# Kernel tuning notes

Measured on AMD Instinct MI355X. Metric: run time of the kernel, lower is better.

## Reference

```python
import jax, jax.numpy as jnp
import numpy as np

N, E, FN, FE, H, B = 8192, 32768, 32, 16, 73, 64
T_MP, T_S2S = 3, 12


def setup_inputs() -> dict:
    key = jax.random.key(0)
    k = jax.random.split(key, 24)
    s = 0.1
    p = lambda i, shape: jax.random.normal(k[i], shape, jnp.float32) * s
    return {
        "node_feats": jax.random.normal(k[0], (N, FN), jnp.float32),
        "edge_feats": jax.random.normal(k[1], (E, FE), jnp.float32),
        "W_in": p(2, (FN, H)), "b_in": p(3, (H,)),
        "ee_W1": p(4, (FE, H)), "ee_b1": p(5, (H,)),
        "ee_W2": p(6, (H, H * H)), "ee_b2": p(7, (H * H,)),
        "gru_Wih": p(8, (3 * H, H)), "gru_Whh": p(9, (3 * H, H)),
        "gru_bih": p(10, (3 * H,)), "gru_bhh": p(11, (3 * H,)),
        "lstm_Wih": p(12, (4 * H, 2 * H)), "lstm_Whh": p(13, (4 * H, H)),
        "lstm_bih": p(14, (4 * H,)), "lstm_bhh": p(15, (4 * H,)),
        "W_out": p(16, (H, 1)), "b_out": p(17, (1,)),
        "Esrc": jax.random.randint(k[18], (E,), 0, N),
        "Etgt": jax.random.randint(k[19], (E,), 0, N),
        "batch": jnp.sort(jax.random.randint(k[20], (N,), 0, B)),
    }


def reference(node_feats, edge_feats, W_in, b_in, ee_W1, ee_b1, ee_W2, ee_b2,
              gru_Wih, gru_Whh, gru_bih, gru_bhh,
              lstm_Wih, lstm_Whh, lstm_bih, lstm_bhh, W_out, b_out,
              Esrc, Etgt, batch):
    # EdgeEncoderMLP: edge features -> per-edge HxH weight matrices (Gilmer edge network)
    A = (jax.nn.relu(edge_feats @ ee_W1 + ee_b1) @ ee_W2 + ee_b2).reshape(E, H, H)
    h = node_feats @ W_in + b_in  # [N, H]

    def mp_step(h, _):
        m = jnp.einsum('eij,ej->ei', A, h[Esrc])           # per-edge matvec (gather-matmul)
        agg = jax.ops.segment_sum(m, Etgt, num_segments=N)  # scatter-add to targets
        # GRUCell update (torch gate order r,z,n)
        gi = agg @ gru_Wih.T + gru_bih
        gh = h @ gru_Whh.T + gru_bhh
        ir, iz, inn = jnp.split(gi, 3, axis=-1)
        hr, hz, hn = jnp.split(gh, 3, axis=-1)
        r = jax.nn.sigmoid(ir + hr)
        z = jax.nn.sigmoid(iz + hz)
        n = jnp.tanh(inn + r * hn)
        return (1.0 - z) * n + z * h, None

    h, _ = jax.lax.scan(mp_step, h, None, length=T_MP)

    # Set2Set pooling with a 1-layer LSTM (torch gate order i,f,g,o)
    def s2s_step(carry, _):
        q_star, hh, cc = carry
        gates = q_star @ lstm_Wih.T + lstm_bih + hh @ lstm_Whh.T + lstm_bhh
        i, f, g, o = jnp.split(gates, 4, axis=-1)
        cc = jax.nn.sigmoid(f) * cc + jax.nn.sigmoid(i) * jnp.tanh(g)
        hh = jax.nn.sigmoid(o) * jnp.tanh(cc)
        q = hh                                              # [B, H]
        e = jnp.sum(h * q[batch], axis=-1)                  # [N] attention logits
        emax = jax.ops.segment_max(e, batch, num_segments=B)
        a = jnp.exp(e - emax[batch])
        a = a / jax.ops.segment_sum(a, batch, num_segments=B)[batch]
        r = jax.ops.segment_sum(a[:, None] * h, batch, num_segments=B)
        return (jnp.concatenate([q, r], axis=-1), hh, cc), None

    init = (jnp.zeros((B, 2 * H), h.dtype), jnp.zeros((B, H), h.dtype),
            jnp.zeros((B, H), h.dtype))
    (q_star, _, _), _ = jax.lax.scan(s2s_step, init, None, length=T_S2S)
    return q_star[:, :H] @ W_out + b_out  # [B, 1]
```

## Files before the change

kernel.cpp:

```cpp
#include <hip/hip_runtime.h>

typedef _Float16 f16;
typedef f16 f16x2 __attribute__((ext_vector_type(2)));
typedef f16 f16x4 __attribute__((ext_vector_type(4)));
typedef f16 f16x8 __attribute__((ext_vector_type(8)));
typedef float f32x4 __attribute__((ext_vector_type(4)));

#define AS1 __attribute__((address_space(1)))
#define AS3 __attribute__((address_space(3)))

#define NN 8192
#define EE 32768

#if __has_builtin(__builtin_amdgcn_fdot2)
#define HAS_FDOT2 1
#else
#define HAS_FDOT2 0
#endif

__device__ __forceinline__ void glds16(const void* g, void* l) {
  __builtin_amdgcn_global_load_lds((const AS1 unsigned int*)g, (AS3 unsigned int*)l, 16, 0, 0);
}
__device__ __forceinline__ void stage_bytes(const void* g, void* s, int nbytes, int tid) {
  const int lane = tid & 63;
  for (int off = tid * 16; off < nbytes; off += 4096)
    glds16((const char*)g + off, (char*)s + (off - lane * 16));
}

__global__ void prep_kernel(
    const float* __restrict__ nf, const float* __restrict__ ef,
    const float* __restrict__ W_in, const float* __restrict__ b_in,
    const float* __restrict__ W1, const float* __restrict__ b1,
    const float* __restrict__ W2, const float* __restrict__ b2,
    const float* __restrict__ gWih, const float* __restrict__ gWhh,
    const float* __restrict__ lWih, const float* __restrict__ lWhh,
    const int* __restrict__ batch, const int* __restrict__ Etgt,
    float* __restrict__ h, f16* __restrict__ hf, f16* __restrict__ ehh,
    f16* __restrict__ W2f, f16* __restrict__ WihT, f16* __restrict__ WhhT,
    f16* __restrict__ Wcat, int* __restrict__ segstarts,
    int* __restrict__ count, int* __restrict__ bucket) {
  int t = blockIdx.x * 256 + threadIdx.x;
  if (t < 786432) {
    int n = t / 96, i = t - n * 96;
    float v = 0.f;
    if (i < 73) {
      v = b_in[i];
      const float* nr = nf + n * 32;
      #pragma unroll
      for (int f = 0; f < 32; ++f) v += nr[f] * W_in[f * 73 + i];
    }
    h[t] = v; hf[t] = (f16)v;
    return;
  }
  t -= 786432;
  if (t < 2621440) {
    int e = t / 80, k = t - e * 80;
    float v;
    if (k < 73) {
      v = b1[k];
      const float* er = ef + e * 16;
      #pragma unroll
      for (int f = 0; f < 16; ++f) v += er[f] * W1[f * 73 + k];
      v = fmaxf(v, 0.f);
    } else v = (k == 73) ? 1.f : 0.f;
    ehh[t] = (f16)v;
    return;
  }
  t -= 2621440;
  if (t < 614400) {
    int kg = t / 7680, r = t - kg * 7680;
    int nt = r / 1536, r2 = r - nt * 1536;
    int ks = r2 / 512, r3 = r2 - ks * 512;
    int l = r3 >> 3, j = r3 & 7;
    int mr = l & 15, q = l >> 4;
    int i = nt * 16 + mr, jj = ks * 32 + q * 8 + j;
    float v = 0.f;
    if (i < 73 && jj < 73) {
      if (kg < 73) v = W2[kg * 5329 + i * 73 + jj];
      else if (kg == 73) v = b2[i * 73 + jj];
    }
    W2f[t] = (f16)v;
    return;
  }
  t -= 614400;
  if (t < 43008) {
    int half = t / 21504, r = t - half * 21504;
    int g = r / 96, k = r - g * 96;
    float v = 0.f;
    if (g < 219 && k < 73) v = half ? gWhh[g * 73 + k] : gWih[g * 73 + k];
    (half ? WhhT : WihT)[r] = (f16)v;
    return;
  }
  t -= 43008;
  if (t < 67744) {
    int g = t / 232, k = t - g * 232;
    float v = 0.f;
    if (k < 73) v = lWih[g * 146 + k];
    else if (k >= 76 && k < 149) v = lWih[g * 146 + (k - 3)];
    else if (k >= 152 && k < 225) v = lWhh[g * 73 + (k - 152)];
    Wcat[t] = (f16)v;
    return;
  }
  t -= 67744;
  if (t < 65) {
    int key = t, lo = 0, hi = NN;
    while (lo < hi) { int mid = (lo + hi) >> 1; if (batch[mid] < key) lo = mid + 1; else hi = mid; }
    segstarts[t] = lo;
    return;
  }
  t -= 65;
  if (t < EE) {
    int tg = Etgt[t];
    int slot = atomicAdd(&count[tg], 1);
    if (slot < 64) bucket[tg * 64 + slot] = t;
  }
}

__global__ __launch_bounds__(256, 2) void vgemm_kernel(
    const f16* __restrict__ ehh, const f16* __restrict__ hf,
    const f16* __restrict__ W2f, const int* __restrict__ Esrc,
    f16* __restrict__ m) {
  __shared__ __align__(16) f16 w2s[2][15360];
  const int tid = threadIdx.x;
  const int bm = blockIdx.x & 127, ksp = blockIdx.x >> 7;
  const int e0 = bm * 256;
  const int kg0 = ksp * 20;
  const int wave = tid >> 6, lane = tid & 63;
  const int q = lane >> 4, mr = lane & 15;

  stage_bytes(W2f + kg0 * 7680, w2s[0], 30720, tid);

  f16x8 hsv[4][3];
  size_t er80[4];
  #pragma unroll
  for (int mt = 0; mt < 4; ++mt) {
    int er = e0 + wave * 64 + mt * 16 + mr;
    int srcn = Esrc[er];
    er80[mt] = (size_t)er * 80;
    #pragma unroll
    for (int ks = 0; ks < 3; ++ks)
      hsv[mt][ks] = *(const f16x8*)(hf + (size_t)srcn * 96 + ks * 32 + q * 8);
  }

  f32x4 zero = {0.f, 0.f, 0.f, 0.f};
  f32x4 acc[4][5];
  #pragma unroll
  for (int mt = 0; mt < 4; ++mt)
    #pragma unroll
    for (int nt = 0; nt < 5; ++nt) acc[mt][nt] = zero;

  for (int ch = 0; ch < 10; ++ch) {
    f16x2 evq[4];
    #pragma unroll
    for (int mt = 0; mt < 4; ++mt)
      evq[mt] = *(const f16x2*)(ehh + er80[mt] + kg0 + ch * 2);
    __syncthreads();
    if (ch + 1 < 10)
      stage_bytes(W2f + (kg0 + (ch + 1) * 2) * 7680, w2s[(ch + 1) & 1], 30720, tid);
    const f16* wb = w2s[ch & 1];
    #pragma unroll
    for (int i = 0; i < 2; ++i) {
      f16x8 af[4][3];
      #pragma unroll
      for (int mt = 0; mt < 4; ++mt) {
        f16 ev = evq[mt][i];
        f16x8 evv = {ev, ev, ev, ev, ev, ev, ev, ev};
        #pragma unroll
        for (int ks = 0; ks < 3; ++ks) af[mt][ks] = hsv[mt][ks] * evv;
      }
      const f16* wbi = wb + i * 7680;
      #pragma unroll
      for (int nt = 0; nt < 5; ++nt) {
        #pragma unroll
        for (int ks = 0; ks < 3; ++ks) {
          f16x8 bf = *(const f16x8*)(wbi + (nt * 3 + ks) * 512 + lane * 8);
          #pragma unroll
          for (int mt = 0; mt < 4; ++mt)
            acc[mt][nt] = __builtin_amdgcn_mfma_f32_16x16x32_f16(af[mt][ks], bf, acc[mt][nt], 0, 0, 0);
        }
      }
    }
  }
  #pragma unroll
  for (int mt = 0; mt < 4; ++mt) {
    #pragma unroll
    for (int reg = 0; reg < 4; ++reg) {
      int er = e0 + wave * 64 + mt * 16 + q * 4 + reg;
      f16* mp = m + (size_t)er * 320 + ksp * 80;
      #pragma unroll
      for (int nt = 0; nt < 5; ++nt)
        mp[nt * 16 + mr] = (f16)acc[mt][nt][reg];
    }
  }
}

__global__ void gather_kernel(const f16* __restrict__ m, const int* __restrict__ count,
                              const int* __restrict__ bucket, f16* __restrict__ aggf) {
  int t = blockIdx.x * 384 + threadIdx.x;
  int n = t / 96, i = t - n * 96;
  float s = 0.f;
  if (i < 80) {
    int cnt = count[n]; if (cnt > 64) cnt = 64;
    const int* bk = bucket + n * 64;
    for (int j = 0; j < cnt; ++j) {
      const f16* mp = m + (size_t)bk[j] * 320;
      s += ((float)mp[i] + (float)mp[80 + i]) + ((float)mp[160 + i] + (float)mp[240 + i]);
    }
  }
  aggf[t] = (f16)s;
}

__global__ __launch_bounds__(256, 1) void grugemm_kernel(
    const f16* __restrict__ aggf, const f16* __restrict__ hf,
    const f16* __restrict__ WihT, const f16* __restrict__ WhhT,
    f16* __restrict__ G) {
  __shared__ __align__(16) f16 As[128 * 96];
  __shared__ __align__(16) f16 Bs[224 * 96];
  const int tid = threadIdx.x;
  const int bz = blockIdx.x >> 6, bm = blockIdx.x & 63;
  const int m0 = bm * 128;
  const f16* A = bz ? hf : aggf;
  const f16* B = bz ? WhhT : WihT;
  f16* out = G + bz * (NN * 224);
  stage_bytes(A + m0 * 96, As, 128 * 96 * 2, tid);
  stage_bytes(B, Bs, 224 * 96 * 2, tid);
  const int wave = tid >> 6, lane = tid & 63, q = lane >> 4, mr = lane & 15;
  __syncthreads();
  f16x8 af[2][3];
  #pragma unroll
  for (int mt = 0; mt < 2; ++mt)
    #pragma unroll
    for (int ks = 0; ks < 3; ++ks)
      af[mt][ks] = *(const f16x8*)(As + (wave * 32 + mt * 16 + mr) * 96 + ks * 32 + q * 8);
  f32x4 zero = {0.f, 0.f, 0.f, 0.f};
  f32x4 acc[2][14];
  #pragma unroll
  for (int mt = 0; mt < 2; ++mt)
    #pragma unroll
    for (int nt = 0; nt < 14; ++nt) acc[mt][nt] = zero;
  #pragma unroll
  for (int nt = 0; nt < 14; ++nt) {
    #pragma unroll
    for (int ks = 0; ks < 3; ++ks) {
      f16x8 bf = *(const f16x8*)(Bs + (nt * 16 + mr) * 96 + ks * 32 + q * 8);
      #pragma unroll
      for (int mt = 0; mt < 2; ++mt)
        acc[mt][nt] = __builtin_amdgcn_mfma_f32_16x16x32_f16(af[mt][ks], bf, acc[mt][nt], 0, 0, 0);
    }
  }
  #pragma unroll
  for (int mt = 0; mt < 2; ++mt)
    #pragma unroll
    for (int reg = 0; reg < 4; ++reg) {
      int row = m0 + wave * 32 + mt * 16 + q * 4 + reg;
      #pragma unroll
      for (int nt = 0; nt < 14; ++nt)
        out[row * 224 + nt * 16 + mr] = (f16)acc[mt][nt][reg];
    }
}

__global__ void gate_kernel(const f16* __restrict__ G, const float* __restrict__ bih,
                            const float* __restrict__ bhh, float* __restrict__ h,
                            f16* __restrict__ hf) {
  int idx = blockIdx.x * 256 + threadIdx.x;
  int n = idx / 73, i = idx - n * 73;
  const f16* g0 = G + n * 224;
  const f16* g1 = G + NN * 224 + n * 224;
  float rr = (float)g0[i] + bih[i] + (float)g1[i] + bhh[i];
  rr = 1.f / (1.f + __expf(-rr));
  float zz = (float)g0[73 + i] + bih[73 + i] + (float)g1[73 + i] + bhh[73 + i];
  zz = 1.f / (1.f + __expf(-zz));
  float nx = (float)g0[146 + i] + bih[146 + i] + rr * ((float)g1[146 + i] + bhh[146 + i]);
  float nn_ = 2.f / (1.f + __expf(-2.f * nx)) - 1.f;
  float hv = h[n * 96 + i];
  float hn = (1.f - zz) * nn_ + zz * hv;
  h[n * 96 + i] = hn;
  hf[n * 96 + i] = (f16)hn;
}

__device__ __forceinline__ float wred_sum(float v) {
  #pragma unroll
  for (int off = 32; off; off >>= 1) v += __shfl_xor(v, off, 64);
  return v;
}
__device__ __forceinline__ float dot8(f16x8 w, f16x8 x, float acc) {
#if HAS_FDOT2
  acc = __builtin_amdgcn_fdot2((f16x2)__builtin_shufflevector(w, w, 0, 1),
                               (f16x2)__builtin_shufflevector(x, x, 0, 1), acc, false);
  acc = __builtin_amdgcn_fdot2((f16x2)__builtin_shufflevector(w, w, 2, 3),
                               (f16x2)__builtin_shufflevector(x, x, 2, 3), acc, false);
  acc = __builtin_amdgcn_fdot2((f16x2)__builtin_shufflevector(w, w, 4, 5),
                               (f16x2)__builtin_shufflevector(x, x, 4, 5), acc, false);
  acc = __builtin_amdgcn_fdot2((f16x2)__builtin_shufflevector(w, w, 6, 7),
                               (f16x2)__builtin_shufflevector(x, x, 6, 7), acc, false);
#else
  #pragma unroll
  for (int e = 0; e < 8; ++e) acc += (float)w[e] * (float)x[e];
#endif
  return acc;
}
__device__ __forceinline__ float dot4(f16x4 w, f16x4 x, float acc) {
#if HAS_FDOT2
  acc = __builtin_amdgcn_fdot2((f16x2)__builtin_shufflevector(w, w, 0, 1),
                               (f16x2)__builtin_shufflevector(x, x, 0, 1), acc, false);
  acc = __builtin_amdgcn_fdot2((f16x2)__builtin_shufflevector(w, w, 2, 3),
                               (f16x2)__builtin_shufflevector(x, x, 2, 3), acc, false);
#else
  #pragma unroll
  for (int e = 0; e < 4; ++e) acc += (float)w[e] * (float)x[e];
#endif
  return acc;
}

#define S2SCAP 256
#define NCAP 190

__global__ __launch_bounds__(512, 2) void s2s_kernel(
    const float* __restrict__ h, const f16* __restrict__ hf,
    const f16* __restrict__ Wcat,
    const float* __restrict__ lbih, const float* __restrict__ lbhh,
    const float* __restrict__ Wout, const float* __restrict__ bout,
    const int* __restrict__ segstarts, float* __restrict__ out) {
  __shared__ __align__(16) f16 hseg[NCAP * 84];
  __shared__ __align__(16) f16 xcat[240];
  __shared__ float hhv[80];
  __shared__ float gatesv[292];
  __shared__ float earr[S2SCAP];
  __shared__ float red[4];
  __shared__ __align__(16) float rpart[19 * 80];
  const int t = threadIdx.x, b = blockIdx.x;
  const int wid = t >> 6, lane = t & 63;

  const int s0 = segstarts[b];
  int segT = segstarts[b + 1] - s0;
  if (segT > S2SCAP) segT = S2SCAP;
  const int c = segT < NCAP ? segT : NCAP;

  if (t < 240) xcat[t] = (f16)0.f;
  if (t < 80) hhv[t] = 0.f;

  for (int r = wid; r < c; r += 8) {
    if (lane < 19) {
      f16x4 v = *(const f16x4*)(hf + (size_t)(s0 + r) * 96 + lane * 4);
      *(f16x4*)(hseg + r * 84 + lane * 4) = v;
    } else if (lane < 21) {
      f16x4 z = {(f16)0.f, (f16)0.f, (f16)0.f, (f16)0.f};
      *(f16x4*)(hseg + r * 84 + 76 + (lane - 19) * 4) = z;
    }
  }

  const bool isg = (t >= 220);
  const int g2 = t - 220;
  float bias = 0.f;
  if (isg) bias = lbih[g2] + lbhh[g2];
  f16x8 wihF[19], whhF[10];
  {
    const f16* wr = Wcat + (size_t)(isg ? g2 : 0) * 232;
    #pragma unroll
    for (int v = 0; v < 19; ++v) wihF[v] = *(const f16x8*)(wr + v * 8);
    #pragma unroll
    for (int v = 0; v < 10; ++v) whhF[v] = *(const f16x8*)(wr + 152 + v * 8);
  }
  const int nc = t / 10, fo = t - nc * 10;
  float creg = 0.f;
  __syncthreads();

  for (int iter = 0; iter < 12; ++iter) {
    if (isg) {
      float a0 = bias, a1 = 0.f, a2 = 0.f, a3 = 0.f;
      #pragma unroll
      for (int v = 0; v < 19; ++v) {
        f16x8 x = *(const f16x8*)(xcat + v * 8);
        int sel = v & 3;
        if (sel == 0) a0 = dot8(wihF[v], x, a0);
        else if (sel == 1) a1 = dot8(wihF[v], x, a1);
        else if (sel == 2) a2 = dot8(wihF[v], x, a2);
        else a3 = dot8(wihF[v], x, a3);
      }
      #pragma unroll
      for (int v = 0; v < 10; ++v) {
        f16x8 x = *(const f16x8*)(xcat + 152 + v * 8);
        int sel = v & 3;
        if (sel == 0) a0 = dot8(whhF[v], x, a0);
        else if (sel == 1) a1 = dot8(whhF[v], x, a1);
        else if (sel == 2) a2 = dot8(whhF[v], x, a2);
        else a3 = dot8(whhF[v], x, a3);
      }
      gatesv[g2] = (a0 + a1) + (a2 + a3);
    }
    __syncthreads();
    if (t < 73) {
      float ig = 1.f / (1.f + __expf(-gatesv[t]));
      float fg = 1.f / (1.f + __expf(-gatesv[73 + t]));
      float gx = gatesv[146 + t];
      float gg = 2.f / (1.f + __expf(-2.f * gx)) - 1.f;
      float og = 1.f / (1.f + __expf(-gatesv[219 + t]));
      creg = fg * creg + ig * gg;
      float cth = 2.f / (1.f + __expf(-2.f * creg)) - 1.f;
      float hh = og * cth;
      hhv[t] = hh;
      xcat[t] = (f16)hh;
      xcat[152 + t] = (f16)hh;
    }
    __syncthreads();
    if (wid < 3) {
      float a = 0.f;
      if (t < c) {
        const f16* hp = hseg + t * 84;
        float e0 = 0.f, e1 = 0.f;
        #pragma unroll
        for (int k = 0; k < 9; ++k) {
          f16x4 h0 = *(const f16x4*)(hp + 8 * k);
          f16x4 h1 = *(const f16x4*)(hp + 8 * k + 4);
          f16x4 x0 = *(const f16x4*)(xcat + 8 * k);
          f16x4 x1 = *(const f16x4*)(xcat + 8 * k + 4);
          e0 = dot4(h0, x0, e0);
          e1 = dot4(h1, x1, e1);
        }
        f16x4 ht = *(const f16x4*)(hp + 72);
        f16x4 xt = *(const f16x4*)(xcat + 72);
        e0 = dot4(ht, xt, e0);
        a = __expf(fminf(e0 + e1, 80.f));
        earr[t] = a;
      }
      float ws = wred_sum(a);
      if (lane == 0) red[wid] = ws;
    }
    if (wid == 0) {
      float fa = 0.f;
      int n = NCAP + lane;
      if (n < segT) {
        const float* hr = h + (size_t)(s0 + n) * 96;
        float e = 0.f;
        for (int i = 0; i < 73; ++i) e += hr[i] * hhv[i];
        fa = __expf(fminf(e, 80.f));
        earr[n] = fa;
      }
      float ws2 = wred_sum(fa);
      if (lane == 0) red[3] = ws2;
    }
    __syncthreads();
    if (t < 190) {
      float r0 = 0.f, r1 = 0.f, r2 = 0.f, r3 = 0.f, r4 = 0.f, r5 = 0.f, r6 = 0.f, r7 = 0.f;
      #pragma unroll
      for (int j = 0; j < 10; ++j) {
        int n = nc * 10 + j;
        if (n < c) {
          float a = earr[n];
          const f16* hp = hseg + n * 84 + fo * 8;
          f16x4 v0 = *(const f16x4*)(hp);
          f16x4 v1 = *(const f16x4*)(hp + 4);
          r0 += a * (float)v0[0]; r1 += a * (float)v0[1];
          r2 += a * (float)v0[2]; r3 += a * (float)v0[3];
          r4 += a * (float)v1[0]; r5 += a * (float)v1[1];
          r6 += a * (float)v1[2]; r7 += a * (float)v1[3];
        }
      }
      if (nc == 18) {
        for (int n = NCAP; n < segT; ++n) {
          float a = earr[n];
          const f16* hp = hf + (size_t)(s0 + n) * 96 + fo * 8;
          f16x4 v0 = *(const f16x4*)(hp);
          f16x4 v1 = *(const f16x4*)(hp + 4);
          r0 += a * (float)v0[0]; r1 += a * (float)v0[1];
          r2 += a * (float)v0[2]; r3 += a * (float)v0[3];
          r4 += a * (float)v1[0]; r5 += a * (float)v1[1];
          r6 += a * (float)v1[2]; r7 += a * (float)v1[3];
        }
      }
      f32x4 wa = {r0, r1, r2, r3}, wb = {r4, r5, r6, r7};
      *(f32x4*)(rpart + nc * 80 + fo * 8) = wa;
      *(f32x4*)(rpart + nc * 80 + fo * 8 + 4) = wb;
    }
    __syncthreads();
    if (t < 80) {
      float S = red[0] + red[1] + red[2] + red[3];
      float invS = (S > 0.f) ? (1.f / S) : 0.f;
      float r = 0.f;
      #pragma unroll
      for (int ch = 0; ch < 19; ++ch) r += rpart[ch * 80 + t];
      if (t < 73) xcat[76 + t] = (f16)(r * invS);
    }
    __syncthreads();
  }
  if (t < 80) gatesv[t] = (t < 73) ? hhv[t] * Wout[t] : 0.f;
  __syncthreads();
  if (t == 0) {
    float a = bout[0];
    for (int i = 0; i < 73; ++i) a += gatesv[i];
    out[b] = a;
  }
}

#define OFF_H      0u
#define OFF_G      3145728u
#define OFF_HF     17825792u
#define OFF_AGGF   19398656u
#define OFF_EHH    20971520u
#define OFF_W2F    26214400u
#define OFF_WIHT   27443200u
#define OFF_WHHT   27486208u
#define OFF_WCAT   27529216u
#define OFF_SEG    27664704u
#define OFF_CNT    27665024u
#define OFF_BKT    27697792u
#define OFF_M      29794944u

extern "C" void kernel_launch(void* const* d_in, const int* in_sizes, int n_in,
                              void* d_out, int out_size, void* d_ws, size_t ws_size,
                              hipStream_t stream) {
  const float* nf   = (const float*)d_in[0];
  const float* ef   = (const float*)d_in[1];
  const float* W_in = (const float*)d_in[2];
  const float* b_in = (const float*)d_in[3];
  const float* W1   = (const float*)d_in[4];
  const float* b1   = (const float*)d_in[5];
  const float* W2   = (const float*)d_in[6];
  const float* b2   = (const float*)d_in[7];
  const float* gWih = (const float*)d_in[8];
  const float* gWhh = (const float*)d_in[9];
  const float* gbih = (const float*)d_in[10];
  const float* gbhh = (const float*)d_in[11];
  const float* lWih = (const float*)d_in[12];
  const float* lWhh = (const float*)d_in[13];
  const float* lbih = (const float*)d_in[14];
  const float* lbhh = (const float*)d_in[15];
  const float* Wout = (const float*)d_in[16];
  const float* bout = (const float*)d_in[17];
  const int* Esrc   = (const int*)d_in[18];
  const int* Etgt   = (const int*)d_in[19];
  const int* batch  = (const int*)d_in[20];

  char* ws = (char*)d_ws;
  float* h    = (float*)(ws + OFF_H);
  f16* G      = (f16*)(ws + OFF_G);
  f16* m      = (f16*)(ws + OFF_M);
  f16* hf     = (f16*)(ws + OFF_HF);
  f16* aggf   = (f16*)(ws + OFF_AGGF);
  f16* ehh    = (f16*)(ws + OFF_EHH);
  f16* W2f    = (f16*)(ws + OFF_W2F);
  f16* WihT   = (f16*)(ws + OFF_WIHT);
  f16* WhhT   = (f16*)(ws + OFF_WHHT);
  f16* Wcat   = (f16*)(ws + OFF_WCAT);
  int* segst  = (int*)(ws + OFF_SEG);
  int* cnt    = (int*)(ws + OFF_CNT);
  int* bkt    = (int*)(ws + OFF_BKT);

  hipMemsetAsync(cnt, 0, NN * sizeof(int), stream);
  prep_kernel<<<16273, 256, 0, stream>>>(nf, ef, W_in, b_in, W1, b1, W2, b2,
                                         gWih, gWhh, lWih, lWhh, batch, Etgt,
                                         h, hf, ehh, W2f, WihT, WhhT, Wcat,
                                         segst, cnt, bkt);
  for (int step = 0; step < 3; ++step) {
    vgemm_kernel<<<512, 256, 0, stream>>>(ehh, hf, W2f, Esrc, m);
    gather_kernel<<<2048, 384, 0, stream>>>(m, cnt, bkt, aggf);
    grugemm_kernel<<<128, 256, 0, stream>>>(aggf, hf, WihT, WhhT, G);
    gate_kernel<<<2336, 256, 0, stream>>>(G, gbih, gbhh, h, hf);
  }
  s2s_kernel<<<64, 512, 0, stream>>>(h, hf, Wcat, lbih, lbhh, Wout, bout, segst,
                                     (float*)d_out);
}
```

Measured before the change: 331.8 us.

## Triple-buffer W2 staging in vgemm and fold LSTM recurrent weights in Set2Set

The vgemm kernel now pads each W2 k-group to 8192 halves and stages one group per step into a three-deep LDS ring. It waits with explicit vmcnt counts and raw barriers instead of __syncthreads, and raises wave priority around the MFMA loop. The per-edge encoder scalars are preloaded into LDS once rather than read from global each chunk. In Set2Set, the code uses the fact that q equals hh to pre-add lstm_Whh into the Wih columns, removing the recurrent dot products, and caches segment h rows in registers for the attention and readout loops. The cost is more LDS, higher register pressure, and reliance on hand-written waitcnt counts being correct.

Measured after the change: 323.7 us. -2.4%, faster.

```diff
diff --git a/kernel.cpp b/kernel.cpp
--- a/kernel.cpp
+++ b/kernel.cpp
@@ -67,22 +67,24 @@
     return;
   }
   t -= 2621440;
-  if (t < 614400) {
-    int kg = t / 7680, r = t - kg * 7680;
-    int nt = r / 1536, r2 = r - nt * 1536;
-    int ks = r2 / 512, r3 = r2 - ks * 512;
-    int l = r3 >> 3, j = r3 & 7;
-    int mr = l & 15, q = l >> 4;
-    int i = nt * 16 + mr, jj = ks * 32 + q * 8 + j;
+  if (t < 655360) {
+    int kg = t / 8192, r = t - kg * 8192;
     float v = 0.f;
-    if (i < 73 && jj < 73) {
-      if (kg < 73) v = W2[kg * 5329 + i * 73 + jj];
-      else if (kg == 73) v = b2[i * 73 + jj];
+    if (r < 7680) {
+      int nt = r / 1536, r2 = r - nt * 1536;
+      int ks = r2 / 512, r3 = r2 - ks * 512;
+      int l = r3 >> 3, j = r3 & 7;
+      int mr = l & 15, q = l >> 4;
+      int i = nt * 16 + mr, jj = ks * 32 + q * 8 + j;
+      if (i < 73 && jj < 73) {
+        if (kg < 73) v = W2[kg * 5329 + i * 73 + jj];
+        else if (kg == 73) v = b2[i * 73 + jj];
+      }
     }
     W2f[t] = (f16)v;
     return;
   }
-  t -= 614400;
+  t -= 655360;
   if (t < 43008) {
     int half = t / 21504, r = t - half * 21504;
     int g = r / 96, k = r - g * 96;
@@ -95,9 +97,8 @@
   if (t < 67744) {
     int g = t / 232, k = t - g * 232;
     float v = 0.f;
-    if (k < 73) v = lWih[g * 146 + k];
+    if (k < 73) v = lWih[g * 146 + k] + lWhh[g * 73 + k];
     else if (k >= 76 && k < 149) v = lWih[g * 146 + (k - 3)];
-    else if (k >= 152 && k < 225) v = lWhh[g * 73 + (k - 152)];
     Wcat[t] = (f16)v;
     return;
   }
@@ -120,7 +121,8 @@
     const f16* __restrict__ ehh, const f16* __restrict__ hf,
     const f16* __restrict__ W2f, const int* __restrict__ Esrc,
     f16* __restrict__ m) {
-  __shared__ __align__(16) f16 w2s[2][15360];
+  __shared__ __align__(16) f16 w2s[3][8192];
+  __shared__ __align__(16) f16 ehsl[256 * 20];
   const int tid = threadIdx.x;
   const int bm = blockIdx.x & 127, ksp = blockIdx.x >> 7;
   const int e0 = bm * 256;
@@ -128,20 +130,21 @@
   const int wave = tid >> 6, lane = tid & 63;
   const int q = lane >> 4, mr = lane & 15;
 
-  stage_bytes(W2f + kg0 * 7680, w2s[0], 30720, tid);
-
+  {
+    const f16* er = ehh + (size_t)(e0 + tid) * 80 + kg0;
+    #pragma unroll
+    for (int p = 0; p < 5; ++p)
+      *(f16x4*)(ehsl + tid * 20 + p * 4) = *(const f16x4*)(er + p * 4);
+  }
   f16x8 hsv[4][3];
-  size_t er80[4];
   #pragma unroll
   for (int mt = 0; mt < 4; ++mt) {
     int er = e0 + wave * 64 + mt * 16 + mr;
     int srcn = Esrc[er];
-    er80[mt] = (size_t)er * 80;
     #pragma unroll
     for (int ks = 0; ks < 3; ++ks)
       hsv[mt][ks] = *(const f16x8*)(hf + (size_t)srcn * 96 + ks * 32 + q * 8);
   }
-
   f32x4 zero = {0.f, 0.f, 0.f, 0.f};
   f32x4 acc[4][5];
   #pragma unroll
@@ -149,37 +152,45 @@
     #pragma unroll
     for (int nt = 0; nt < 5; ++nt) acc[mt][nt] = zero;
 
-  for (int ch = 0; ch < 10; ++ch) {
-    f16x2 evq[4];
+  __syncthreads();
+  stage_bytes(W2f + (size_t)kg0 * 8192, w2s[0], 16384, tid);
+
+  int rd = 0;
+  for (int ch = 0; ch < 20; ++ch) {
+    if (ch < 19) {
+      int wr = rd + 1; if (wr == 3) wr = 0;
+      stage_bytes(W2f + (size_t)(kg0 + ch + 1) * 8192, w2s[wr], 16384, tid);
+      asm volatile("s_waitcnt vmcnt(4)" ::: "memory");
+    } else {
+      asm volatile("s_waitcnt vmcnt(0)" ::: "memory");
+    }
+    __builtin_amdgcn_s_barrier();
+    const f16* wb = w2s[rd];
+    f16 ev[4];
     #pragma unroll
     for (int mt = 0; mt < 4; ++mt)
-      evq[mt] = *(const f16x2*)(ehh + er80[mt] + kg0 + ch * 2);
-    __syncthreads();
-    if (ch + 1 < 10)
-      stage_bytes(W2f + (kg0 + (ch + 1) * 2) * 7680, w2s[(ch + 1) & 1], 30720, tid);
-    const f16* wb = w2s[ch & 1];
-    #pragma unroll
-    for (int i = 0; i < 2; ++i) {
-      f16x8 af[4][3];
-      #pragma unroll
-      for (int mt = 0; mt < 4; ++mt) {
-        f16 ev = evq[mt][i];
-        f16x8 evv = {ev, ev, ev, ev, ev, ev, ev, ev};
+      ev[mt] = ehsl[(wave * 64 + mt * 16 + mr) * 20 + ch];
+    f16x8 af[4][3];
+    #pragma unroll
+    for (int mt = 0; mt < 4; ++mt) {
+      f16 e = ev[mt];
+      f16x8 evv = {e, e, e, e, e, e, e, e};
+      #pragma unroll
+      for (int ks = 0; ks < 3; ++ks) af[mt][ks] = hsv[mt][ks] * evv;
+    }
+    __builtin_amdgcn_s_setprio(1);
+    #pragma unroll
+    for (int nt = 0; nt < 5; ++nt) {
+      #pragma unroll
+      for (int ks = 0; ks < 3; ++ks) {
+        f16x8 bf = *(const f16x8*)(wb + (nt * 3 + ks) * 512 + lane * 8);
         #pragma unroll
-        for (int ks = 0; ks < 3; ++ks) af[mt][ks] = hsv[mt][ks] * evv;
-      }
-      const f16* wbi = wb + i * 7680;
-      #pragma unroll
-      for (int nt = 0; nt < 5; ++nt) {
-        #pragma unroll
-        for (int ks = 0; ks < 3; ++ks) {
-          f16x8 bf = *(const f16x8*)(wbi + (nt * 3 + ks) * 512 + lane * 8);
-          #pragma unroll
-          for (int mt = 0; mt < 4; ++mt)
-            acc[mt][nt] = __builtin_amdgcn_mfma_f32_16x16x32_f16(af[mt][ks], bf, acc[mt][nt], 0, 0, 0);
-        }
-      }
-    }
+        for (int mt = 0; mt < 4; ++mt)
+          acc[mt][nt] = __builtin_amdgcn_mfma_f32_16x16x32_f16(af[mt][ks], bf, acc[mt][nt], 0, 0, 0);
+      }
+    }
+    __builtin_amdgcn_s_setprio(0);
+    rd = rd + 1; if (rd == 3) rd = 0;
   }
   #pragma unroll
   for (int mt = 0; mt < 4; ++mt) {
@@ -338,14 +349,14 @@
 
   if (t < 240) xcat[t] = (f16)0.f;
   if (t < 80) hhv[t] = 0.f;
-
-  for (int r = wid; r < c; r += 8) {
-    if (lane < 19) {
-      f16x4 v = *(const f16x4*)(hf + (size_t)(s0 + r) * 96 + lane * 4);
+  if (t < S2SCAP) earr[t] = 0.f;
+
+  for (int r = wid; r < NCAP; r += 8) {
+    if (lane < 21) {
+      f16x4 v = {(f16)0.f, (f16)0.f, (f16)0.f, (f16)0.f};
+      if (r < c && lane < 19)
+        v = *(const f16x4*)(hf + (size_t)(s0 + r) * 96 + lane * 4);
       *(f16x4*)(hseg + r * 84 + lane * 4) = v;
-    } else if (lane < 21) {
-      f16x4 z = {(f16)0.f, (f16)0.f, (f16)0.f, (f16)0.f};
-      *(f16x4*)(hseg + r * 84 + 76 + (lane - 19) * 4) = z;
     }
   }
 
@@ -353,17 +364,32 @@
   const int g2 = t - 220;
   float bias = 0.f;
   if (isg) bias = lbih[g2] + lbhh[g2];
-  f16x8 wihF[19], whhF[10];
+  f16x8 wihF[19];
   {
     const f16* wr = Wcat + (size_t)(isg ? g2 : 0) * 232;
     #pragma unroll
     for (int v = 0; v < 19; ++v) wihF[v] = *(const f16x8*)(wr + v * 8);
-    #pragma unroll
-    for (int v = 0; v < 10; ++v) whhF[v] = *(const f16x8*)(wr + 152 + v * 8);
   }
   const int nc = t / 10, fo = t - nc * 10;
   float creg = 0.f;
   __syncthreads();
+
+  f16x4 hrow[19];
+  {
+    const f16* hp = hseg + (t < NCAP ? t : 0) * 84;
+    #pragma unroll
+    for (int k = 0; k < 19; ++k) hrow[k] = *(const f16x4*)(hp + k * 4);
+  }
+  f16x4 hb0[10], hb1[10];
+  {
+    int ncc = (t < 190) ? nc : 0, foc = (t < 190) ? fo : 0;
+    #pragma unroll
+    for (int j = 0; j < 10; ++j) {
+      const f16* hp = hseg + (ncc * 10 + j) * 84 + foc * 8;
+      hb0[j] = *(const f16x4*)(hp);
+      hb1[j] = *(const f16x4*)(hp + 4);
+    }
+  }
 
   for (int iter = 0; iter < 12; ++iter) {
     if (isg) {
@@ -376,15 +402,6 @@
         else if (sel == 1) a1 = dot8(wihF[v], x, a1);
         else if (sel == 2) a2 = dot8(wihF[v], x, a2);
         else a3 = dot8(wihF[v], x, a3);
-      }
-      #pragma unroll
-      for (int v = 0; v < 10; ++v) {
-        f16x8 x = *(const f16x8*)(xcat + 152 + v * 8);
-        int sel = v & 3;
-        if (sel == 0) a0 = dot8(whhF[v], x, a0);
-        else if (sel == 1) a1 = dot8(whhF[v], x, a1);
-        else if (sel == 2) a2 = dot8(whhF[v], x, a2);
-        else a3 = dot8(whhF[v], x, a3);
       }
       gatesv[g2] = (a0 + a1) + (a2 + a3);
     }
@@ -400,26 +417,18 @@
       float hh = og * cth;
       hhv[t] = hh;
       xcat[t] = (f16)hh;
-      xcat[152 + t] = (f16)hh;
     }
     __syncthreads();
     if (wid < 3) {
       float a = 0.f;
       if (t < c) {
-        const f16* hp = hseg + t * 84;
         float e0 = 0.f, e1 = 0.f;
         #pragma unroll
-        for (int k = 0; k < 9; ++k) {
-          f16x4 h0 = *(const f16x4*)(hp + 8 * k);
-          f16x4 h1 = *(const f16x4*)(hp + 8 * k + 4);
-          f16x4 x0 = *(const f16x4*)(xcat + 8 * k);
-          f16x4 x1 = *(const f16x4*)(xcat + 8 * k + 4);
-          e0 = dot4(h0, x0, e0);
-          e1 = dot4(h1, x1, e1);
+        for (int k = 0; k < 19; ++k) {
+          f16x4 xk = *(const f16x4*)(xcat + k * 4);
+          if (k & 1) e1 = dot4(hrow[k], xk, e1);
+          else e0 = dot4(hrow[k], xk, e0);
         }
-        f16x4 ht = *(const f16x4*)(hp + 72);
-        f16x4 xt = *(const f16x4*)(xcat + 72);
-        e0 = dot4(ht, xt, e0);
         a = __expf(fminf(e0 + e1, 80.f));
         earr[t] = a;
       }
@@ -444,17 +453,11 @@
       float r0 = 0.f, r1 = 0.f, r2 = 0.f, r3 = 0.f, r4 = 0.f, r5 = 0.f, r6 = 0.f, r7 = 0.f;
       #pragma unroll
       for (int j = 0; j < 10; ++j) {
-        int n = nc * 10 + j;
-        if (n < c) {
-          float a = earr[n];
-          const f16* hp = hseg + n * 84 + fo * 8;
-          f16x4 v0 = *(const f16x4*)(hp);
-          f16x4 v1 = *(const f16x4*)(hp + 4);
-          r0 += a * (float)v0[0]; r1 += a * (float)v0[1];
-          r2 += a * (float)v0[2]; r3 += a * (float)v0[3];
-          r4 += a * (float)v1[0]; r5 += a * (float)v1[1];
-          r6 += a * (float)v1[2]; r7 += a * (float)v1[3];
-        }
+        float a = earr[nc * 10 + j];
+        r0 += a * (float)hb0[j][0]; r1 += a * (float)hb0[j][1];
+        r2 += a * (float)hb0[j][2]; r3 += a * (float)hb0[j][3];
+        r4 += a * (float)hb1[j][0]; r5 += a * (float)hb1[j][1];
+        r6 += a * (float)hb1[j][2]; r7 += a * (float)hb1[j][3];
       }
       if (nc == 18) {
         for (int n = NCAP; n < segT; ++n) {
@@ -498,13 +501,13 @@
 #define OFF_AGGF   19398656u
 #define OFF_EHH    20971520u
 #define OFF_W2F    26214400u
-#define OFF_WIHT   27443200u
-#define OFF_WHHT   27486208u
-#define OFF_WCAT   27529216u
-#define OFF_SEG    27664704u
-#define OFF_CNT    27665024u
-#define OFF_BKT    27697792u
-#define OFF_M      29794944u
+#define OFF_WIHT   27525120u
+#define OFF_WHHT   27568128u
+#define OFF_WCAT   27611136u
+#define OFF_SEG    27746624u
+#define OFF_CNT    27747072u
+#define OFF_BKT    27779840u
+#define OFF_M      29877248u
 
 extern "C" void kernel_launch(void* const* d_in, const int* in_sizes, int n_in,
                               void* d_out, int out_size, void* d_ws, size_t ws_size,
@@ -534,7 +537,6 @@
   char* ws = (char*)d_ws;
   float* h    = (float*)(ws + OFF_H);
   f16* G      = (f16*)(ws + OFF_G);
-  f16* m      = (f16*)(ws + OFF_M);
   f16* hf     = (f16*)(ws + OFF_HF);
   f16* aggf   = (f16*)(ws + OFF_AGGF);
   f16* ehh    = (f16*)(ws + OFF_EHH);
@@ -545,9 +547,10 @@
   int* segst  = (int*)(ws + OFF_SEG);
   int* cnt    = (int*)(ws + OFF_CNT);
   int* bkt    = (int*)(ws + OFF_BKT);
+  f16* m      = (f16*)(ws + OFF_M);
 
   hipMemsetAsync(cnt, 0, NN * sizeof(int), stream);
-  prep_kernel<<<16273, 256, 0, stream>>>(nf, ef, W_in, b_in, W1, b1, W2, b2,
+  prep_kernel<<<16433, 256, 0, stream>>>(nf, ef, W_in, b_in, W1, b1, W2, b2,
                                          gWih, gWhh, lWih, lWhh, batch, Etgt,
                                          h, hf, ehh, W2f, WihT, WhhT, Wcat,
                                          segst, cnt, bkt);
```
